# Kernel optimization log

Hardware: AMD Instinct MI355X
Metric: run time of the kernel (lower is better)

Reference implementation:

```python
import jax, jax.numpy as jnp
import numpy as np

B, N, A = 2, 4096, 5
TOPK = 30
K_RBF = 16
MAX_AA = 22
MAXREL = 32
EDGE_IN = 16 + K_RBF * 25 + 14 + 16  # 446
EDGE_FEAT = 128
PI = 3.1415926


def l2norm(v, eps=1e-12):
    n = jnp.sqrt(jnp.sum(v * v, axis=-1, keepdims=True))
    return v / jnp.maximum(n, eps)


def gather_nodes(nodes, idx):
    # nodes: (B,N,C), idx: (B,N,K) -> (B,N,K,C)
    b, n, k = idx.shape
    flat = idx.reshape(b, n * k, 1)
    out = jnp.take_along_axis(nodes, flat, axis=1)
    return out.reshape(b, n, k, nodes.shape[-1])


def quaternions(R):
    # R: (...,3,3) -> unit quaternion (...,4)
    Rxx, Ryy, Rzz = R[..., 0, 0], R[..., 1, 1], R[..., 2, 2]
    mag = 0.5 * jnp.sqrt(jnp.abs(1.0 + jnp.stack([Rxx - Ryy - Rzz, -Rxx + Ryy - Rzz, -Rxx - Ryy + Rzz], -1)) + 1e-12)
    signs = jnp.sign(jnp.stack([R[..., 2, 1] - R[..., 1, 2], R[..., 0, 2] - R[..., 2, 0], R[..., 1, 0] - R[..., 0, 1]], -1))
    xyz = signs * mag
    w = jnp.sqrt(jax.nn.relu(1.0 + Rxx + Ryy + Rzz) + 1e-12)[..., None] / 2.0
    return l2norm(jnp.concatenate([xyz, w], -1))


def setup_inputs():
    key = jax.random.key(0)
    ks = jax.random.split(key, 12)
    X = jax.random.normal(ks[0], (B, N, A, 3), jnp.float32) * 3.0
    mask = jnp.ones((B, N), jnp.float32)
    mask_atoms = jnp.ones((B, N, A), jnp.float32)
    means = jax.random.normal(ks[1], (K_RBF,), jnp.float32)
    stds = jax.random.normal(ks[2], (K_RBF,), jnp.float32)
    mul_w = jax.random.normal(ks[3], (A * A,), jnp.float32)
    bias_w = jax.random.normal(ks[4], (A * A,), jnp.float32)
    aa_pair_embed = jax.random.normal(ks[5], (MAX_AA * MAX_AA, K_RBF), jnp.float32) * 0.02
    aa_pair_embed = aa_pair_embed.at[441].set(0.0)  # padding_idx
    relpos_embed = jax.random.normal(ks[6], (2 * MAXREL + 1, 16), jnp.float32) * 0.02
    mask_embed = jax.random.normal(ks[7], (2, 16), jnp.float32) * 0.02
    W1 = jax.random.normal(ks[8], (EDGE_IN, EDGE_IN), jnp.float32) / np.sqrt(EDGE_IN)
    b1 = jnp.zeros((EDGE_IN,), jnp.float32)
    W2 = jax.random.normal(ks[9], (EDGE_IN, EDGE_FEAT), jnp.float32) / np.sqrt(EDGE_IN)
    b2 = jnp.zeros((EDGE_FEAT,), jnp.float32)
    aa = jax.random.randint(ks[10], (B, N), 0, 21, jnp.int32)
    residue_idx = jnp.tile(jnp.arange(N, dtype=jnp.int32)[None, :], (B, 1))
    chain_labels = jax.random.randint(ks[11], (B, N), 0, 2, jnp.int32)
    return dict(X=X, mask=mask, mask_atoms=mask_atoms, means=means, stds=stds, mul_w=mul_w,
                bias_w=bias_w, aa_pair_embed=aa_pair_embed, relpos_embed=relpos_embed,
                mask_embed=mask_embed, W1=W1, b1=b1, W2=W2, b2=b2, aa=aa,
                residue_idx=residue_idx, chain_labels=chain_labels)


def reference(X, mask, mask_atoms, means, stds, mul_w, bias_w, aa_pair_embed, relpos_embed,
              mask_embed, W1, b1, W2, b2, aa, residue_idx, chain_labels):
    Ca = X[:, :, 1]  # (B,N,3) C-alpha
    # ---- _dist: spatial kNN over C-alpha ----
    mask2d = mask[:, :, None] * mask[:, None, :]
    dx = Ca[:, None, :, :] - Ca[:, :, None, :]
    D = mask2d * jnp.sqrt(jnp.sum(dx * dx, -1) + 1e-6)
    D_adj = D + (1.0 - mask2d) * jnp.max(D, -1, keepdims=True)
    _, E_idx = jax.lax.top_k(-D_adj, TOPK)  # smallest distances
    mask_attend = jnp.take_along_axis(mask2d, E_idx, axis=2)  # (B,N,K)
    # ---- orientation features (local frames + quaternions) ----
    ones3 = jnp.ones((B, 1, 3), X.dtype)
    u = l2norm(jnp.concatenate([ones3, Ca[:, 1:] - Ca[:, :-1]], 1))
    b_ = l2norm(jnp.concatenate([u[:, :-1] - u[:, 1:], ones3], 1))
    n_ = l2norm(jnp.concatenate([jnp.cross(u[:, :-1], u[:, 1:]), ones3], 1))
    lf = jnp.stack([b_, n_, jnp.cross(b_, n_)], axis=2)  # (B,N,3,3)
    X_nb = gather_nodes(Ca, E_idx)                       # (B,N,K,3)
    O_nb = gather_nodes(lf.reshape(B, N, 9), E_idx).reshape(B, N, TOPK, 3, 3)
    t = X_nb - Ca[:, :, None, :]
    t = jnp.einsum('bnij,bnkj->bnki', lf, t)
    t = l2norm(t) * mask_attend[..., None]
    r = jnp.einsum('bnji,bnkjl->bnkil', lf, O_nb)  # lf^T @ O_nb
    q = quaternions(r) * mask_attend[..., None]
    O_feat = jnp.concatenate([t, q, 1.0 - 2.0 * jnp.abs(t), 1.0 - 2.0 * jnp.abs(q)], -1)  # (B,N,K,14)
    # ---- positional / chain embeddings ----
    offset = residue_idx[:, :, None] - residue_idx[:, None, :]
    offset_nb = jnp.take_along_axis(offset, E_idx, 2)
    d_chain = (chain_labels[:, :, None] == chain_labels[:, None, :]).astype(jnp.int32)
    E_chains = jnp.take_along_axis(d_chain, E_idx, 2)
    d = jnp.clip(offset_nb + MAXREL, 0, 2 * MAXREL)
    E_pos = relpos_embed[d] + mask_embed[E_chains]  # (B,N,K,16)
    # ---- GaussianLayer: aa-pair embed + atom-pair distance RBF ----
    aa_pair = aa[:, :, None] * MAX_AA + aa[:, None, :]
    aa_nb = jnp.take_along_axis(aa_pair, E_idx, 2)
    feat_aapair = aa_pair_embed[aa_nb] * mask_attend[..., None]  # (B,N,K,16)
    nbX = gather_nodes(X.reshape(B, N, A * 3), E_idx).reshape(B, N, TOPK, A, 3)
    delta = nbX[:, :, :, :, None, :] - X[:, :, None, None, :, :]  # (B,N,K,A,A,3)
    Dab = jnp.sqrt(jnp.sum(delta * delta, -1) + 1e-12)            # (B,N,K,A,A)
    et = jnp.arange(A * A).reshape(A, A)
    xg = mul_w[et] * Dab + bias_w[et]
    m_nb = gather_nodes(mask_atoms, E_idx)  # (B,N,K,A)
    xg = xg * (m_nb[..., None, :] * m_nb[..., :, None])
    std = jnp.abs(stds) + 0.01
    g = jnp.exp(-0.5 * ((xg[..., None] - means) / std) ** 2) / ((2.0 * PI) ** 0.5 * std)
    gbf = g.reshape(B, N, TOPK, A * A * K_RBF) * mask_attend[..., None]  # (B,N,K,400)
    # ---- fuse and project (NonLinear gbf_proj) ----
    E = jnp.concatenate([E_pos, gbf, O_feat, feat_aapair], -1)  # (B,N,K,446)
    h = jax.nn.gelu(E @ W1 + b1, approximate=False)
    return h @ W2 + b2  # (B,N,K,128)
```

## Files before the change

### kernel.cpp

```cpp
#include <hip/hip_runtime.h>
#include <cstdint>
#include <cstddef>

#define NN 4096
#define TOPK_ 30
#define BN_TOT 8192
#define M_TOT 245760
#define KP 448
#define HSTRIDE 136
#define EF 128

typedef unsigned short u16;
typedef unsigned int u32;
typedef __attribute__((ext_vector_type(8))) short bf16x8;
typedef __attribute__((ext_vector_type(4))) float f32x4;

__device__ __forceinline__ float b2f(u16 u){ return __uint_as_float(((u32)u)<<16); }
__device__ __forceinline__ u16 f2b(float f){
  u32 u = __float_as_uint(f);
  return (u16)((u + 0x7FFFu + ((u>>16)&1u)) >> 16);
}
__device__ __forceinline__ float ldf(const void* p, long i, int fl){
  return fl ? ((const float*)p)[i] : b2f(((const u16*)p)[i]);
}
__device__ __forceinline__ int is_f32_flag(const u16* mask){
  return (((const u32*)mask)[0] == 0x3F800000u) ? 1 : 0;
}
__device__ __forceinline__ void norm3(float x,float y,float z,float&ox,float&oy,float&oz){
  float n = sqrtf(x*x+y*y+z*z); n = fmaxf(n, 1e-12f);
  ox=x/n; oy=y/n; oz=z/n;
}
__device__ __forceinline__ float sgn(float x){ return x>0.f?1.f:(x<0.f?-1.f:0.f); }
__device__ __forceinline__ float gelu_fast(float x){
  float y = 0.70710678118654752440f * x;
  float s = fabsf(y);
  float t = __builtin_amdgcn_rcpf(fmaf(0.3275911f, s, 1.0f));
  float p = fmaf(fmaf(fmaf(fmaf(1.061405429f, t, -1.453152027f), t, 1.421413741f), t,
                 -0.284496736f), t, 0.254829592f);
  float e = __expf(-y*y);
  float erfs = fmaf(-p*t, e, 1.0f);
  float erfy = (x >= 0.f) ? erfs : -erfs;
  float hx = 0.5f*x;
  return fmaf(hx, erfy, hx);
}
__device__ __forceinline__ u32 pk_bf16(float lo, float hi){
  u32 r;
  asm("v_cvt_pk_bf16_f32 %0, %1, %2" : "=v"(r) : "v"(lo), "v"(hi));
  return r;
}
__device__ __forceinline__ void ld16(const void* p, int row, int fl, float* o){
  if (fl) {
    const float4* q = (const float4*)((const float*)p + (long)row*16);
    float4 a=q[0], b=q[1], c=q[2], d=q[3];
    o[0]=a.x; o[1]=a.y; o[2]=a.z; o[3]=a.w;
    o[4]=b.x; o[5]=b.y; o[6]=b.z; o[7]=b.w;
    o[8]=c.x; o[9]=c.y; o[10]=c.z; o[11]=c.w;
    o[12]=d.x; o[13]=d.y; o[14]=d.z; o[15]=d.w;
  } else {
    const uint4* q = (const uint4*)((const u16*)p + (long)row*16);
    uint4 a=q[0], b=q[1];
    o[0]=__uint_as_float(a.x<<16);  o[1]=__uint_as_float(a.x&0xFFFF0000u);
    o[2]=__uint_as_float(a.y<<16);  o[3]=__uint_as_float(a.y&0xFFFF0000u);
    o[4]=__uint_as_float(a.z<<16);  o[5]=__uint_as_float(a.z&0xFFFF0000u);
    o[6]=__uint_as_float(a.w<<16);  o[7]=__uint_as_float(a.w&0xFFFF0000u);
    o[8]=__uint_as_float(b.x<<16);  o[9]=__uint_as_float(b.x&0xFFFF0000u);
    o[10]=__uint_as_float(b.y<<16); o[11]=__uint_as_float(b.y&0xFFFF0000u);
    o[12]=__uint_as_float(b.z<<16); o[13]=__uint_as_float(b.z&0xFFFF0000u);
    o[14]=__uint_as_float(b.w<<16); o[15]=__uint_as_float(b.w&0xFFFF0000u);
  }
}

__global__ __launch_bounds__(256) void prep_kernel(
    const void* __restrict__ X, const u16* __restrict__ mask,
    const void* __restrict__ mask_atoms,
    const void* __restrict__ means, const void* __restrict__ stds,
    const void* __restrict__ mul_w, const void* __restrict__ bias_w,
    const void* __restrict__ W1, const void* __restrict__ b1,
    const void* __restrict__ W2, const void* __restrict__ b2,
    float* __restrict__ ca, float* __restrict__ lf,
    u16* __restrict__ W1P, u16* __restrict__ W2P,
    float* __restrict__ b1p, float* __restrict__ b2p,
    float* __restrict__ Fp, float* __restrict__ wsc)
{
  const int fl = is_f32_flag(mask);
  int idx = blockIdx.x*256 + threadIdx.x;
  if (idx < BN_TOT) {
    int i = idx & (NN-1);
    float xr[15];
    #pragma unroll
    for (int v = 0; v < 15; ++v) xr[v] = ldf(X, (long)idx*15+v, fl);
    float cax = xr[3], cay = xr[4], caz = xr[5];
    ca[idx*4+0]=cax; ca[idx*4+1]=cay; ca[idx*4+2]=caz; ca[idx*4+3]=0.f;
    {
      float mres = ldf(mask, idx, fl);
      float m0 = ldf(mask_atoms,(long)idx*5+0,fl), m1 = ldf(mask_atoms,(long)idx*5+1,fl);
      float m2 = ldf(mask_atoms,(long)idx*5+2,fl), m3 = ldf(mask_atoms,(long)idx*5+3,fl);
      float m4 = ldf(mask_atoms,(long)idx*5+4,fl);
      float4* F4 = (float4*)(Fp + (long)idx*24);
      F4[0] = make_float4(xr[0],xr[1],xr[2],xr[3]);
      F4[1] = make_float4(xr[4],xr[5],xr[6],xr[7]);
      F4[2] = make_float4(xr[8],xr[9],xr[10],xr[11]);
      F4[3] = make_float4(xr[12],xr[13],xr[14],mres);
      F4[4] = make_float4(m0,m1,m2,m3);
      F4[5] = make_float4(m4,0.f,0.f,0.f);
    }
    float bx,by,bz,nx,ny,nz;
    if (i < NN-1) {
      float uix,uiy,uiz;
      if (i==0) { norm3(1.f,1.f,1.f,uix,uiy,uiz); }
      else {
        float px=ldf(X,(long)(idx-1)*15+3,fl), py=ldf(X,(long)(idx-1)*15+4,fl), pz=ldf(X,(long)(idx-1)*15+5,fl);
        norm3(cax-px, cay-py, caz-pz, uix,uiy,uiz);
      }
      float qx=ldf(X,(long)(idx+1)*15+3,fl), qy=ldf(X,(long)(idx+1)*15+4,fl), qz=ldf(X,(long)(idx+1)*15+5,fl);
      float vx,vy,vz; norm3(qx-cax, qy-cay, qz-caz, vx,vy,vz);
      norm3(uix-vx, uiy-vy, uiz-vz, bx,by,bz);
      norm3(uiy*vz-uiz*vy, uiz*vx-uix*vz, uix*vy-uiy*vx, nx,ny,nz);
    } else {
      norm3(1.f,1.f,1.f,bx,by,bz); nx=bx; ny=by; nz=bz;
    }
    float cx = by*nz - bz*ny, cy = bz*nx - bx*nz, cz = bx*ny - by*nx;
    float* L = lf + (size_t)idx*12;
    L[0]=bx;L[1]=by;L[2]=bz;L[3]=nx;L[4]=ny;L[5]=nz;L[6]=cx;L[7]=cy;L[8]=cz;
    return;
  }
  int r1 = idx - BN_TOT;
  if (r1 < 229376) {
    int f = r1 >> 9, li = r1 & 511;
    int n0 = f / 14, kc = f - n0*14;
    int ln = li >> 3, j = li & 7;
    int n = n0*16 + (ln & 15);
    int k = kc*32 + (ln >> 4)*8 + j;
    W1P[r1] = (n < 446 && k < 446) ? (fl ? f2b(((const float*)W1)[(long)k*446 + n])
                                         : ((const u16*)W1)[(long)k*446 + n]) : (u16)0;
    return;
  }
  int r2 = r1 - 229376;
  if (r2 < 65536) {
    int f = r2 >> 9, li = r2 & 511;
    int n0 = f >> 4, kc = f & 15;
    int ln = li >> 3, j = li & 7;
    int n = n0*16 + (ln & 15);
    int k = kc*32 + (ln >> 4)*8 + j;
    W2P[r2] = (k < 446) ? (fl ? f2b(((const float*)W2)[(long)k*128 + n])
                              : ((const u16*)W2)[(long)k*128 + n]) : (u16)0;
    return;
  }
  int r3 = r2 - 65536;
  if (r3 < 512) { b1p[r3] = (r3<446)? ldf(b1, r3, fl) : 0.f; return; }
  int r4 = r3 - 512;
  if (r4 < 128) { b2p[r4] = ldf(b2, r4, fl); return; }
  int r5 = r4 - 128;
  if (r5 < 16) {
    float sd = fabsf(ldf(stds, r5, fl)) + 0.01f;
    float ri = 1.0f / sd;
    wsc[r5] = ldf(means, r5, fl);
    wsc[16 + r5] = ri;
    wsc[32 + r5] = 0.3989422804014327f * ri;
    return;
  }
  if (r5 < 41) { wsc[48 + (r5-16)] = ldf(mul_w, r5-16, fl); return; }
  if (r5 < 66) { wsc[73 + (r5-41)] = ldf(bias_w, r5-41, fl); }
}

__global__ __launch_bounds__(64) void knn_kernel(const float4* __restrict__ ca,
                                                 int* __restrict__ eidx)
{
#pragma clang fp contract(off)
  __shared__ u32 keys[64*65];
  int bi = blockIdx.x;
  int lane = threadIdx.x;
  int b = bi >> 12;
  const float4 ci = ca[bi];
  const float4* cab = ca + (b<<12);
  u32 mind = 0xFFFFFFFFu; int minj = 1<<30;
  for (int c = 0; c < 64; ++c) {
    int j = (c<<6) | lane;
    float4 cj = cab[j];
    float dx = cj.x-ci.x, dy = cj.y-ci.y, dz = cj.z-ci.z;
    float ss = dx*dx;
    ss = ss + dy*dy;
    ss = ss + dz*dz;
    float d = sqrtf(ss + 1e-6f);
    u32 db = __float_as_uint(d);
    keys[lane*65 + c] = db;
    if (db < mind) { mind = db; minj = j; }
  }
  __syncthreads();
  for (int r = 0; r < TOPK_; ++r) {
    u32 wd = mind; int wj = minj;
    #pragma unroll
    for (int off = 32; off; off >>= 1) {
      u32 od = __shfl_xor(wd, off, 64);
      int oj = __shfl_xor(wj, off, 64);
      if (od < wd || (od == wd && oj < wj)) { wd = od; wj = oj; }
    }
    if (lane == 0) eidx[bi*TOPK_ + r] = wj;
    int wl = wj & 63;
    if (lane == wl) keys[wl*65 + (wj>>6)] = 0xFFFFFFFFu;
    __syncthreads();
    u32 kv = keys[wl*65 + lane];
    int kj = (lane<<6)|wl;
    #pragma unroll
    for (int off = 32; off; off >>= 1) {
      u32 od = __shfl_xor(kv, off, 64);
      int oj = __shfl_xor(kj, off, 64);
      if (od < kv || (od == kv && oj < kj)) { kv = od; kj = oj; }
    }
    if (lane == wl) { mind = kv; minj = kj; }
  }
}

__global__ __launch_bounds__(512,2) void mega_mlp(
    const float* __restrict__ Fp, const float* __restrict__ wsc,
    const u16* __restrict__ mask,
    const void* __restrict__ aa_pe, const void* __restrict__ relpos, const void* __restrict__ mask_emb,
    const int* __restrict__ aa, const int* __restrict__ ridx, const int* __restrict__ chains,
    const int* __restrict__ eidx, const float* __restrict__ ca, const float* __restrict__ lf,
    const u16* __restrict__ W1P, const u16* __restrict__ W2P,
    const float* __restrict__ b1p, const float* __restrict__ b2p,
    void* __restrict__ C)
{
  __shared__ __align__(16) u16 Et[128*448];
  __shared__ float Dabs[128][29];
  __shared__ float maA[128];
  const int fl = is_f32_flag(mask);
  int tid = threadIdx.x;
  int lane = tid & 63, wave = tid >> 6;
  int wr = wave >> 2, wc = wave & 3;
  int rowBase = blockIdx.x * 128;

  {
    int eo = tid >> 2, q = tid & 3;
    int e = rowBase + eo;
    int bi = (int)((unsigned)e / 30u);
    int k = e - bi*30;
    int bj = ((bi >> 12) << 12) + eidx[bi*TOPK_ + k];
    const float* Fi = Fp + (long)bi*24;
    const float* Fj = Fp + (long)bj*24;
    float Xi[15];
    {
      const float4* F4 = (const float4*)Fi;
      float4 A=F4[0], B=F4[1], Cc=F4[2], D=F4[3];
      Xi[0]=A.x;Xi[1]=A.y;Xi[2]=A.z;Xi[3]=A.w;
      Xi[4]=B.x;Xi[5]=B.y;Xi[6]=B.z;Xi[7]=B.w;
      Xi[8]=Cc.x;Xi[9]=Cc.y;Xi[10]=Cc.z;Xi[11]=Cc.w;
      Xi[12]=D.x;Xi[13]=D.y;Xi[14]=D.z;
      if (q == 1) maA[eo] = D.w * Fj[15];
    }
    float4 Mj = *(const float4*)(Fj + 16);
    float  Mj4 = Fj[20];
    for (int a = q; a < 5; a += 4) {
      float xj0 = Fj[a*3+0], xj1 = Fj[a*3+1], xj2 = Fj[a*3+2];
      float mja = Fj[16+a];
      #pragma unroll
      for (int c = 0; c < 5; ++c) {
        float d0 = xj0 - Xi[c*3+0];
        float d1 = xj1 - Xi[c*3+1];
        float d2 = xj2 - Xi[c*3+2];
        float Dab = sqrtf(d0*d0 + d1*d1 + d2*d2 + 1e-12f);
        float mjc = (c==0)?Mj.x:(c==1)?Mj.y:(c==2)?Mj.z:(c==3)?Mj.w:Mj4;
        float mw = wsc[48 + a*5+c], bw = wsc[73 + a*5+c];
        Dabs[eo][a*5+c] = (mw*Dab + bw) * (mja * mjc);
      }
    }
  }

  if (tid < 128) {
    int eo = tid;
    int e = rowBase + eo;
    int bi = (int)((unsigned)e / 30u);
    int k = e - bi*30;
    int bj = ((bi >> 12) << 12) + eidx[bi*TOPK_ + k];
    float ma = Fp[(long)bi*24+15] * Fp[(long)bj*24+15];
    char* rowB = (char*)Et + eo*896;
    int xr = (eo & 7) << 4;
    {
      int d = ridx[bi] - ridx[bj] + 32; d = d < 0 ? 0 : (d > 64 ? 64 : d);
      int ch = (chains[bi] == chains[bj]) ? 1 : 0;
      float rp[16], me[16];
      ld16(relpos, d, fl, rp);
      ld16(mask_emb, ch, fl, me);
      uint4 wA, wB;
      wA.x = pk_bf16(rp[0]+me[0],  rp[1]+me[1]);
      wA.y = pk_bf16(rp[2]+me[2],  rp[3]+me[3]);
      wA.z = pk_bf16(rp[4]+me[4],  rp[5]+me[5]);
      wA.w = pk_bf16(rp[6]+me[6],  rp[7]+me[7]);
      wB.x = pk_bf16(rp[8]+me[8],  rp[9]+me[9]);
      wB.y = pk_bf16(rp[10]+me[10],rp[11]+me[11]);
      wB.z = pk_bf16(rp[12]+me[12],rp[13]+me[13]);
      wB.w = pk_bf16(rp[14]+me[14],rp[15]+me[15]);
      *(uint4*)(rowB + (0 ^ xr))  = wA;
      *(uint4*)(rowB + (16 ^ xr)) = wB;
    }
    float t0,t1,t2,q0,q1,q2,qw;
    {
      float Li[9], Lj[9];
      {
        const float4* L4 = (const float4*)(lf + (size_t)bi*12);
        float4 a=L4[0], b=L4[1], c=L4[2];
        Li[0]=a.x;Li[1]=a.y;Li[2]=a.z;Li[3]=a.w;Li[4]=b.x;Li[5]=b.y;Li[6]=b.z;Li[7]=b.w;Li[8]=c.x;
        const float4* M4 = (const float4*)(lf + (size_t)bj*12);
        float4 d=M4[0], e2=M4[1], f=M4[2];
        Lj[0]=d.x;Lj[1]=d.y;Lj[2]=d.z;Lj[3]=d.w;Lj[4]=e2.x;Lj[5]=e2.y;Lj[6]=e2.z;Lj[7]=e2.w;Lj[8]=f.x;
      }
      float4 ci = *(const float4*)(ca + bj*4);
      float4 c0 = *(const float4*)(ca + bi*4);
      float dx = ci.x-c0.x, dy = ci.y-c0.y, dz = ci.z-c0.z;
      t0 = Li[0]*dx+Li[1]*dy+Li[2]*dz;
      t1 = Li[3]*dx+Li[4]*dy+Li[5]*dz;
      t2 = Li[6]*dx+Li[7]*dy+Li[8]*dz;
      float tn = fmaxf(sqrtf(t0*t0+t1*t1+t2*t2), 1e-12f);
      t0 = t0/tn*ma; t1 = t1/tn*ma; t2 = t2/tn*ma;
      float R00=Li[0]*Lj[0]+Li[3]*Lj[3]+Li[6]*Lj[6];
      float R01=Li[0]*Lj[1]+Li[3]*Lj[4]+Li[6]*Lj[7];
      float R02=Li[0]*Lj[2]+Li[3]*Lj[5]+Li[6]*Lj[8];
      float R10=Li[1]*Lj[0]+Li[4]*Lj[3]+Li[7]*Lj[6];
      float R11=Li[1]*Lj[1]+Li[4]*Lj[4]+Li[7]*Lj[7];
      float R12=Li[1]*Lj[2]+Li[4]*Lj[5]+Li[7]*Lj[8];
      float R20=Li[2]*Lj[0]+Li[5]*Lj[3]+Li[8]*Lj[6];
      float R21=Li[2]*Lj[1]+Li[5]*Lj[4]+Li[8]*Lj[7];
      float R22=Li[2]*Lj[2]+Li[5]*Lj[5]+Li[8]*Lj[8];
      float m0 = 0.5f*sqrtf(fabsf(1.f+R00-R11-R22)+1e-12f);
      float m1 = 0.5f*sqrtf(fabsf(1.f-R00+R11-R22)+1e-12f);
      float m2 = 0.5f*sqrtf(fabsf(1.f-R00-R11+R22)+1e-12f);
      q0 = sgn(R21-R12)*m0; q1 = sgn(R02-R20)*m1; q2 = sgn(R10-R01)*m2;
      qw = 0.5f*sqrtf(fmaxf(1.f+R00+R11+R22, 0.f)+1e-12f);
      float qn = fmaxf(sqrtf(q0*q0+q1*q1+q2*q2+qw*qw), 1e-12f);
      q0 = q0/qn*ma; q1 = q1/qn*ma; q2 = q2/qn*ma; qw = qw/qn*ma;
    }
    {
      int aap = aa[bi]*22 + aa[bj];
      float av[16];
      ld16(aa_pe, aap, fl, av);
      uint4 w0, w1, w2, w3;
      w0.x = pk_bf16(t0, t1);  w0.y = pk_bf16(t2, q0);
      w0.z = pk_bf16(q1, q2);  w0.w = pk_bf16(qw, 1.f-2.f*fabsf(t0));
      w1.x = pk_bf16(1.f-2.f*fabsf(t1), 1.f-2.f*fabsf(t2));
      w1.y = pk_bf16(1.f-2.f*fabsf(q0), 1.f-2.f*fabsf(q1));
      w1.z = pk_bf16(1.f-2.f*fabsf(q2), 1.f-2.f*fabsf(qw));
      w1.w = pk_bf16(av[0]*ma, av[1]*ma);
      w2.x = pk_bf16(av[2]*ma, av[3]*ma);   w2.y = pk_bf16(av[4]*ma, av[5]*ma);
      w2.z = pk_bf16(av[6]*ma, av[7]*ma);   w2.w = pk_bf16(av[8]*ma, av[9]*ma);
      w3.x = pk_bf16(av[10]*ma, av[11]*ma); w3.y = pk_bf16(av[12]*ma, av[13]*ma);
      w3.z = pk_bf16(av[14]*ma, av[15]*ma); w3.w = 0u;
      *(uint4*)(rowB + (832 ^ xr)) = w0;
      *(uint4*)(rowB + (848 ^ xr)) = w1;
      *(uint4*)(rowB + (864 ^ xr)) = w2;
      *(uint4*)(rowB + (880 ^ xr)) = w3;
    }
  }
  __syncthreads();

  {
    float meanv[16], rinvv[16], coefv[16];
    {
      const float4* W4 = (const float4*)wsc;
      #pragma unroll
      for (int g = 0; g < 4; ++g) {
        float4 m = W4[g], r = W4[4+g], c = W4[8+g];
        meanv[g*4+0]=m.x; meanv[g*4+1]=m.y; meanv[g*4+2]=m.z; meanv[g*4+3]=m.w;
        rinvv[g*4+0]=r.x; rinvv[g*4+1]=r.y; rinvv[g*4+2]=r.z; rinvv[g*4+3]=r.w;
        coefv[g*4+0]=c.x; coefv[g*4+1]=c.y; coefv[g*4+2]=c.z; coefv[g*4+3]=c.w;
      }
    }
    #pragma unroll 1
    for (int i = 0; i < 13; ++i) {
      int G = tid + i*512;
      if (G < 6400) {
        int row = (int)((unsigned)G / 50u);
        int gp = G - row*50;
        float xg = Dabs[row][gp >> 1];
        float ma = maA[row];
        int odd = gp & 1;
        u32 w[4];
        #pragma unroll
        for (int j2 = 0; j2 < 4; ++j2) {
          float me0 = odd ? meanv[j2*2+8] : meanv[j2*2];
          float ri0 = odd ? rinvv[j2*2+8] : rinvv[j2*2];
          float co0 = odd ? coefv[j2*2+8] : coefv[j2*2];
          float me1 = odd ? meanv[j2*2+9] : meanv[j2*2+1];
          float ri1 = odd ? rinvv[j2*2+9] : rinvv[j2*2+1];
          float co1 = odd ? coefv[j2*2+9] : coefv[j2*2+1];
          float z0 = (xg - me0) * ri0;
          float z1 = (xg - me1) * ri1;
          float v0 = __expf(-0.5f*z0*z0) * co0 * ma;
          float v1 = __expf(-0.5f*z1*z1) * co1 * ma;
          w[j2] = pk_bf16(v0, v1);
        }
        uint4 W4o; W4o.x = w[0]; W4o.y = w[1]; W4o.z = w[2]; W4o.w = w[3];
        *(uint4*)((char*)Et + row*896 + ((32 + (gp<<4)) ^ ((row&7)<<4))) = W4o;
      }
    }
  }
  __syncthreads();

  u32 hpk[4][4][2][2];
  #define GEMM1_HALF(H) do {                                                      \
    f32x4 acc1h[2][4][2] = {};                                                    \
    _Pragma("unroll 1")                                                           \
    for (int t = 0; t < 7; ++t) {                                                 \
      bf16x8 af[2][4];                                                            \
      _Pragma("unroll")                                                           \
      for (int kk = 0; kk < 2; ++kk)                                              \
        _Pragma("unroll")                                                         \
        for (int r = 0; r < 4; ++r) {                                             \
          int row = wr*64 + r*16 + (lane&15);                                     \
          int s = kk*4 + (lane>>4);                                               \
          af[kk][r] = *(const bf16x8*)(Et + row*448 + t*64 + ((s ^ (row&7))<<3)); \
        }                                                                         \
      bf16x8 bg[2][2][2];                                                         \
      _Pragma("unroll")                                                           \
      for (int c = 0; c < 2; ++c)                                                 \
        _Pragma("unroll")                                                         \
        for (int cc = 0; cc < 2; ++cc)                                            \
          _Pragma("unroll")                                                       \
          for (int kk = 0; kk < 2; ++kk)                                          \
            bg[c][cc][kk] = *(const bf16x8*)(W1P +                                \
              ((((2*(H)+c)*8 + wc*2 + cc)*14 + t*2 + kk) << 9) + lane*8);         \
      _Pragma("unroll")                                                           \
      for (int c = 0; c < 2; ++c)                                                 \
        _Pragma("unroll")                                                         \
        for (int r = 0; r < 4; ++r)                                               \
          _Pragma("unroll")                                                       \
          for (int cc = 0; cc < 2; ++cc)                                          \
            _Pragma("unroll")                                                     \
            for (int kk = 0; kk < 2; ++kk)                                        \
              acc1h[c][r][cc] = __builtin_amdgcn_mfma_f32_16x16x32_bf16(          \
                  af[kk][r], bg[c][cc][kk], acc1h[c][r][cc], 0,0,0);              \
    }                                                                             \
    _Pragma("unroll")                                                             \
    for (int c = 0; c < 2; ++c)                                                   \
      _Pragma("unroll")                                                           \
      for (int r = 0; r < 4; ++r)                                                 \
        _Pragma("unroll")                                                         \
        for (int cc = 0; cc < 2; ++cc) {                                          \
          int col = wc*32 + cc*16 + (lane & 15);                                  \
          float bv = b1p[(2*(H)+c)*128 + col];                                    \
          hpk[2*(H)+c][r][cc][0] = pk_bf16(gelu_fast(acc1h[c][r][cc][0]+bv),      \
                                           gelu_fast(acc1h[c][r][cc][1]+bv));     \
          hpk[2*(H)+c][r][cc][1] = pk_bf16(gelu_fast(acc1h[c][r][cc][2]+bv),      \
                                           gelu_fast(acc1h[c][r][cc][3]+bv));     \
        }                                                                         \
  } while(0)

  GEMM1_HALF(0);
  GEMM1_HALF(1);
  #undef GEMM1_HALF

  u16* hs0 = Et;
  u16* hs1 = Et + 128*HSTRIDE;
  #define STORE_HS(cN, buf) do {                                                  \
    _Pragma("unroll")                                                             \
    for (int r = 0; r < 4; ++r) {                                                 \
      _Pragma("unroll")                                                           \
      for (int cc = 0; cc < 2; ++cc) {                                            \
        int col = wc*32 + cc*16 + (lane & 15);                                    \
        int row0 = wr*64 + r*16 + (lane>>4)*4;                                    \
        u32 p01 = hpk[cN][r][cc][0], p23 = hpk[cN][r][cc][1];                     \
        u16* hb_ = (buf) + row0*HSTRIDE + col;                                    \
        hb_[0]         = (u16)p01; hb_[HSTRIDE]   = (u16)(p01>>16);               \
        hb_[2*HSTRIDE] = (u16)p23; hb_[3*HSTRIDE] = (u16)(p23>>16);               \
      }                                                                           \
    }                                                                             \
  } while(0)

  f32x4 acc2[4][2] = {};
  __syncthreads();
  STORE_HS(0, hs0);
  __syncthreads();
  #pragma unroll
  for (int c = 0; c < 4; ++c) {
    u16* hb = (c & 1) ? hs1 : hs0;
    u16* hn = (c & 1) ? hs0 : hs1;
    if (c < 3) STORE_HS(c+1, hn);
    #pragma unroll
    for (int k2 = 0; k2 < 4; ++k2) {
      bf16x8 af2[4], bg2[2];
      #pragma unroll
      for (int r = 0; r < 4; ++r) {
        int row = wr*64 + r*16 + (lane&15);
        af2[r] = *(const bf16x8*)(hb + row*HSTRIDE + k2*32 + (lane>>4)*8);
      }
      #pragma unroll
      for (int cc = 0; cc < 2; ++cc)
        bg2[cc] = *(const bf16x8*)(W2P + ((((wc*2+cc)*16) + c*4 + k2) << 9) + lane*8);
      #pragma unroll
      for (int r = 0; r < 4; ++r)
        #pragma unroll
        for (int cc = 0; cc < 2; ++cc)
          acc2[r][cc] = __builtin_amdgcn_mfma_f32_16x16x32_bf16(af2[r], bg2[cc], acc2[r][cc], 0,0,0);
    }
    __syncthreads();
  }
  #undef STORE_HS

  const int f32out = fl;
  #pragma unroll
  for (int r = 0; r < 4; ++r) {
    #pragma unroll
    for (int cc = 0; cc < 2; ++cc) {
      int col = wc*32 + cc*16 + (lane & 15);
      float bv = b2p[col];
      #pragma unroll
      for (int g = 0; g < 4; ++g) {
        long row = (long)rowBase + wr*64 + r*16 + (lane>>4)*4 + g;
        float v = acc2[r][cc][g] + bv;
        long o = row*EF + col;
        if (f32out) ((float*)C)[o] = v;
        else        ((u16*)C)[o]  = f2b(v);
      }
    }
  }
}

extern "C" void kernel_launch(void* const* d_in, const int* in_sizes, int n_in,
                              void* d_out, int out_size, void* d_ws, size_t ws_size,
                              hipStream_t stream) {
  const void* X          = d_in[0];
  const u16* mask        = (const u16*)d_in[1];
  const void* mask_atoms = d_in[2];
  const void* means      = d_in[3];
  const void* stds       = d_in[4];
  const void* mul_w      = d_in[5];
  const void* bias_w     = d_in[6];
  const void* aa_pe      = d_in[7];
  const void* relpos     = d_in[8];
  const void* mask_emb   = d_in[9];
  const void* W1         = d_in[10];
  const void* b1         = d_in[11];
  const void* W2         = d_in[12];
  const void* b2         = d_in[13];
  const int* aa          = (const int*)d_in[14];
  const int* ridx        = (const int*)d_in[15];
  const int* chains      = (const int*)d_in[16];

  char* ws = (char*)d_ws;
  float* ca  = (float*)(ws + 0);
  float* lf  = (float*)(ws + 131072);
  int* eidx  = (int*)(ws + 524288);
  u16* W1P   = (u16*)(ws + 1507328);
  u16* W2P   = (u16*)(ws + 1966080);
  float* b1p = (float*)(ws + 2097152);
  float* b2p = (float*)(ws + 2099200);
  float* wsc = (float*)(ws + 2099712);
  float* Fp  = (float*)(ws + 2100224);

  prep_kernel<<<1187, 256, 0, stream>>>(X, mask, mask_atoms, means, stds, mul_w, bias_w,
                                        W1, b1, W2, b2, ca, lf, W1P, W2P, b1p, b2p, Fp, wsc);
  knn_kernel<<<BN_TOT, 64, 0, stream>>>((const float4*)ca, eidx);
  mega_mlp<<<M_TOT/128, 512, 0, stream>>>(Fp, wsc, mask,
                                          aa_pe, relpos, mask_emb, aa, ridx, chains,
                                          eidx, ca, lf, W1P, W2P, b1p, b2p, d_out);
}
```

Baseline: 673.3 us.

## Halve MLP row tile to 64 with 256-thread blocks and coalesced weight repack

The fused MLP kernel now processes 64 edge rows per block with 4 waves in a 2x2 arrangement instead of 128 rows with 8 waves. Each wave now covers 32 rows by 64 columns, so it loads more weight fragments per MFMA and fewer activation fragments. LDS use per block is halved, which lets more blocks fit on each CU. The prep kernel's weight repacking now indexes threads by the source (k,n) order, so global reads are coalesced and writes are scattered. The trade-off is twice as many blocks, each reading the full W1/W2 from global/L2, which raises weight traffic per output row.

```diff
diff --git a/kernel.cpp b/kernel.cpp
--- a/kernel.cpp
+++ b/kernel.cpp
@@ -9,6 +9,7 @@
 #define KP 448
 #define HSTRIDE 136
 #define EF 128
+#define BR 64
 
 typedef unsigned short u16;
 typedef unsigned int u32;
@@ -126,24 +127,22 @@
   }
   int r1 = idx - BN_TOT;
   if (r1 < 229376) {
-    int f = r1 >> 9, li = r1 & 511;
-    int n0 = f / 14, kc = f - n0*14;
-    int ln = li >> 3, j = li & 7;
-    int n = n0*16 + (ln & 15);
-    int k = kc*32 + (ln >> 4)*8 + j;
-    W1P[r1] = (n < 446 && k < 446) ? (fl ? f2b(((const float*)W1)[(long)k*446 + n])
-                                         : ((const u16*)W1)[(long)k*446 + n]) : (u16)0;
+    int k = r1 >> 9, n = r1 & 511;
+    u16 v = (n < 446 && k < 446) ? (fl ? f2b(((const float*)W1)[(long)k*446 + n])
+                                       : ((const u16*)W1)[(long)k*446 + n]) : (u16)0;
+    int frag = (n >> 4)*14 + (k >> 5);
+    int li = ((n & 15) + 16*((k & 31) >> 3))*8 + (k & 7);
+    W1P[(frag << 9) + li] = v;
     return;
   }
   int r2 = r1 - 229376;
   if (r2 < 65536) {
-    int f = r2 >> 9, li = r2 & 511;
-    int n0 = f >> 4, kc = f & 15;
-    int ln = li >> 3, j = li & 7;
-    int n = n0*16 + (ln & 15);
-    int k = kc*32 + (ln >> 4)*8 + j;
-    W2P[r2] = (k < 446) ? (fl ? f2b(((const float*)W2)[(long)k*128 + n])
-                              : ((const u16*)W2)[(long)k*128 + n]) : (u16)0;
+    int k = r2 >> 7, n = r2 & 127;
+    u16 v = (k < 446) ? (fl ? f2b(((const float*)W2)[(long)k*128 + n])
+                            : ((const u16*)W2)[(long)k*128 + n]) : (u16)0;
+    int frag = (n >> 4)*16 + (k >> 5);
+    int li = ((n & 15) + 16*((k & 31) >> 3))*8 + (k & 7);
+    W2P[(frag << 9) + li] = v;
     return;
   }
   int r3 = r2 - 65536;
@@ -211,7 +210,7 @@
   }
 }
 
-__global__ __launch_bounds__(512,2) void mega_mlp(
+__global__ __launch_bounds__(256,2) void mega_mlp(
     const float* __restrict__ Fp, const float* __restrict__ wsc,
     const u16* __restrict__ mask,
     const void* __restrict__ aa_pe, const void* __restrict__ relpos, const void* __restrict__ mask_emb,
@@ -221,14 +220,14 @@
     const float* __restrict__ b1p, const float* __restrict__ b2p,
     void* __restrict__ C)
 {
-  __shared__ __align__(16) u16 Et[128*448];
-  __shared__ float Dabs[128][29];
-  __shared__ float maA[128];
+  __shared__ __align__(16) u16 Et[BR*448];
+  __shared__ float Dabs[BR][29];
+  __shared__ float maA[BR];
   const int fl = is_f32_flag(mask);
   int tid = threadIdx.x;
   int lane = tid & 63, wave = tid >> 6;
-  int wr = wave >> 2, wc = wave & 3;
-  int rowBase = blockIdx.x * 128;
+  int wr = wave >> 1, wc = wave & 1;
+  int rowBase = blockIdx.x * BR;
 
   {
     int eo = tid >> 2, q = tid & 3;
@@ -266,7 +265,7 @@
     }
   }
 
-  if (tid < 128) {
+  if (tid < BR) {
     int eo = tid;
     int e = rowBase + eo;
     int bi = (int)((unsigned)e / 30u);
@@ -295,32 +294,27 @@
     }
     float t0,t1,t2,q0,q1,q2,qw;
     {
-      float Li[9], Lj[9];
-      {
-        const float4* L4 = (const float4*)(lf + (size_t)bi*12);
-        float4 a=L4[0], b=L4[1], c=L4[2];
-        Li[0]=a.x;Li[1]=a.y;Li[2]=a.z;Li[3]=a.w;Li[4]=b.x;Li[5]=b.y;Li[6]=b.z;Li[7]=b.w;Li[8]=c.x;
-        const float4* M4 = (const float4*)(lf + (size_t)bj*12);
-        float4 d=M4[0], e2=M4[1], f=M4[2];
-        Lj[0]=d.x;Lj[1]=d.y;Lj[2]=d.z;Lj[3]=d.w;Lj[4]=e2.x;Lj[5]=e2.y;Lj[6]=e2.z;Lj[7]=e2.w;Lj[8]=f.x;
-      }
-      float4 ci = *(const float4*)(ca + bj*4);
-      float4 c0 = *(const float4*)(ca + bi*4);
-      float dx = ci.x-c0.x, dy = ci.y-c0.y, dz = ci.z-c0.z;
-      t0 = Li[0]*dx+Li[1]*dy+Li[2]*dz;
-      t1 = Li[3]*dx+Li[4]*dy+Li[5]*dz;
-      t2 = Li[6]*dx+Li[7]*dy+Li[8]*dz;
+      const float4* L4i = (const float4*)(lf + (size_t)bi*12);
+      float4 a0=L4i[0], a1=L4i[1], a2=L4i[2];
+      const float4* L4j = (const float4*)(lf + (size_t)bj*12);
+      float4 b0=L4j[0], b1v=L4j[1], b2v=L4j[2];
+      float4 cj4 = *(const float4*)(ca + bj*4);
+      float4 ci4 = *(const float4*)(ca + bi*4);
+      float dx = cj4.x-ci4.x, dy = cj4.y-ci4.y, dz = cj4.z-ci4.z;
+      t0 = a0.x*dx + a0.y*dy + a0.z*dz;
+      t1 = a0.w*dx + a1.x*dy + a1.y*dz;
+      t2 = a1.z*dx + a1.w*dy + a2.x*dz;
       float tn = fmaxf(sqrtf(t0*t0+t1*t1+t2*t2), 1e-12f);
       t0 = t0/tn*ma; t1 = t1/tn*ma; t2 = t2/tn*ma;
-      float R00=Li[0]*Lj[0]+Li[3]*Lj[3]+Li[6]*Lj[6];
-      float R01=Li[0]*Lj[1]+Li[3]*Lj[4]+Li[6]*Lj[7];
-      float R02=Li[0]*Lj[2]+Li[3]*Lj[5]+Li[6]*Lj[8];
-      float R10=Li[1]*Lj[0]+Li[4]*Lj[3]+Li[7]*Lj[6];
-      float R11=Li[1]*Lj[1]+Li[4]*Lj[4]+Li[7]*Lj[7];
-      float R12=Li[1]*Lj[2]+Li[4]*Lj[5]+Li[7]*Lj[8];
-      float R20=Li[2]*Lj[0]+Li[5]*Lj[3]+Li[8]*Lj[6];
-      float R21=Li[2]*Lj[1]+Li[5]*Lj[4]+Li[8]*Lj[7];
-      float R22=Li[2]*Lj[2]+Li[5]*Lj[5]+Li[8]*Lj[8];
+      float R00 = a0.x*b0.x + a0.w*b0.w + a1.z*b1v.z;
+      float R01 = a0.x*b0.y + a0.w*b1v.x + a1.z*b1v.w;
+      float R02 = a0.x*b0.z + a0.w*b1v.y + a1.z*b2v.x;
+      float R10 = a0.y*b0.x + a1.x*b0.w + a1.w*b1v.z;
+      float R11 = a0.y*b0.y + a1.x*b1v.x + a1.w*b1v.w;
+      float R12 = a0.y*b0.z + a1.x*b1v.y + a1.w*b2v.x;
+      float R20 = a0.z*b0.x + a1.y*b0.w + a2.x*b1v.z;
+      float R21 = a0.z*b0.y + a1.y*b1v.x + a2.x*b1v.w;
+      float R22 = a0.z*b0.z + a1.y*b1v.y + a2.x*b2v.x;
       float m0 = 0.5f*sqrtf(fabsf(1.f+R00-R11-R22)+1e-12f);
       float m1 = 0.5f*sqrtf(fabsf(1.f-R00+R11-R22)+1e-12f);
       float m2 = 0.5f*sqrtf(fabsf(1.f-R00-R11+R22)+1e-12f);
@@ -366,8 +360,8 @@
     }
     #pragma unroll 1
     for (int i = 0; i < 13; ++i) {
-      int G = tid + i*512;
-      if (G < 6400) {
+      int G = tid + i*256;
+      if (G < 3200) {
         int row = (int)((unsigned)G / 50u);
         int gp = G - row*50;
         float xg = Dabs[row][gp >> 1];
@@ -395,47 +389,46 @@
   }
   __syncthreads();
 
-  u32 hpk[4][4][2][2];
+  u32 hpk[4][2][4][2];
   #define GEMM1_HALF(H) do {                                                      \
-    f32x4 acc1h[2][4][2] = {};                                                    \
+    f32x4 acc1h[2][2][4] = {};                                                    \
     _Pragma("unroll 1")                                                           \
     for (int t = 0; t < 7; ++t) {                                                 \
-      bf16x8 af[2][4];                                                            \
+      bf16x8 af[2][2];                                                            \
       _Pragma("unroll")                                                           \
       for (int kk = 0; kk < 2; ++kk)                                              \
         _Pragma("unroll")                                                         \
-        for (int r = 0; r < 4; ++r) {                                             \
-          int row = wr*64 + r*16 + (lane&15);                                     \
+        for (int r = 0; r < 2; ++r) {                                             \
+          int row = wr*32 + r*16 + (lane&15);                                     \
           int s = kk*4 + (lane>>4);                                               \
           af[kk][r] = *(const bf16x8*)(Et + row*448 + t*64 + ((s ^ (row&7))<<3)); \
         }                                                                         \
-      bf16x8 bg[2][2][2];                                                         \
       _Pragma("unroll")                                                           \
-      for (int c = 0; c < 2; ++c)                                                 \
+      for (int c = 0; c < 2; ++c) {                                               \
+        bf16x8 bg[4][2];                                                          \
         _Pragma("unroll")                                                         \
-        for (int cc = 0; cc < 2; ++cc)                                            \
+        for (int cc = 0; cc < 4; ++cc)                                            \
           _Pragma("unroll")                                                       \
           for (int kk = 0; kk < 2; ++kk)                                          \
-            bg[c][cc][kk] = *(const bf16x8*)(W1P +                                \
-              ((((2*(H)+c)*8 + wc*2 + cc)*14 + t*2 + kk) << 9) + lane*8);         \
-      _Pragma("unroll")                                                           \
-      for (int c = 0; c < 2; ++c)                                                 \
+            bg[cc][kk] = *(const bf16x8*)(W1P +                                   \
+              ((((2*(H)+c)*8 + wc*4 + cc)*14 + t*2 + kk) << 9) + lane*8);         \
         _Pragma("unroll")                                                         \
-        for (int r = 0; r < 4; ++r)                                               \
+        for (int r = 0; r < 2; ++r)                                               \
           _Pragma("unroll")                                                       \
-          for (int cc = 0; cc < 2; ++cc)                                          \
+          for (int cc = 0; cc < 4; ++cc)                                          \
             _Pragma("unroll")                                                     \
             for (int kk = 0; kk < 2; ++kk)                                        \
               acc1h[c][r][cc] = __builtin_amdgcn_mfma_f32_16x16x32_bf16(          \
-                  af[kk][r], bg[c][cc][kk], acc1h[c][r][cc], 0,0,0);              \
+                  af[kk][r], bg[cc][kk], acc1h[c][r][cc], 0,0,0);                 \
+      }                                                                           \
     }                                                                             \
     _Pragma("unroll")                                                             \
     for (int c = 0; c < 2; ++c)                                                   \
       _Pragma("unroll")                                                           \
-      for (int r = 0; r < 4; ++r)                                                 \
+      for (int r = 0; r < 2; ++r)                                                 \
         _Pragma("unroll")                                                         \
-        for (int cc = 0; cc < 2; ++cc) {                                          \
-          int col = wc*32 + cc*16 + (lane & 15);                                  \
+        for (int cc = 0; cc < 4; ++cc) {                                          \
+          int col = wc*64 + cc*16 + (lane & 15);                                  \
           float bv = b1p[(2*(H)+c)*128 + col];                                    \
           hpk[2*(H)+c][r][cc][0] = pk_bf16(gelu_fast(acc1h[c][r][cc][0]+bv),      \
                                            gelu_fast(acc1h[c][r][cc][1]+bv));     \
@@ -449,14 +442,14 @@
   #undef GEMM1_HALF
 
   u16* hs0 = Et;
-  u16* hs1 = Et + 128*HSTRIDE;
+  u16* hs1 = Et + BR*HSTRIDE;
   #define STORE_HS(cN, buf) do {                                                  \
     _Pragma("unroll")                                                             \
-    for (int r = 0; r < 4; ++r) {                                                 \
+    for (int r = 0; r < 2; ++r) {                                                 \
       _Pragma("unroll")                                                           \
-      for (int cc = 0; cc < 2; ++cc) {                                            \
-        int col = wc*32 + cc*16 + (lane & 15);                                    \
-        int row0 = wr*64 + r*16 + (lane>>4)*4;                                    \
+      for (int cc = 0; cc < 4; ++cc) {                                            \
+        int col = wc*64 + cc*16 + (lane & 15);                                    \
+        int row0 = wr*32 + r*16 + (lane>>4)*4;                                    \
         u32 p01 = hpk[cN][r][cc][0], p23 = hpk[cN][r][cc][1];                     \
         u16* hb_ = (buf) + row0*HSTRIDE + col;                                    \
         hb_[0]         = (u16)p01; hb_[HSTRIDE]   = (u16)(p01>>16);               \
@@ -465,7 +458,7 @@
     }                                                                             \
   } while(0)
 
-  f32x4 acc2[4][2] = {};
+  f32x4 acc2[2][4] = {};
   __syncthreads();
   STORE_HS(0, hs0);
   __syncthreads();
@@ -476,19 +469,19 @@
     if (c < 3) STORE_HS(c+1, hn);
     #pragma unroll
     for (int k2 = 0; k2 < 4; ++k2) {
-      bf16x8 af2[4], bg2[2];
+      bf16x8 af2[2], bg2[4];
       #pragma unroll
-      for (int r = 0; r < 4; ++r) {
-        int row = wr*64 + r*16 + (lane&15);
+      for (int r = 0; r < 2; ++r) {
+        int row = wr*32 + r*16 + (lane&15);
         af2[r] = *(const bf16x8*)(hb + row*HSTRIDE + k2*32 + (lane>>4)*8);
       }
       #pragma unroll
-      for (int cc = 0; cc < 2; ++cc)
-        bg2[cc] = *(const bf16x8*)(W2P + ((((wc*2+cc)*16) + c*4 + k2) << 9) + lane*8);
+      for (int cc = 0; cc < 4; ++cc)
+        bg2[cc] = *(const bf16x8*)(W2P + ((((wc*4+cc)*16) + c*4 + k2) << 9) + lane*8);
       #pragma unroll
-      for (int r = 0; r < 4; ++r)
+      for (int r = 0; r < 2; ++r)
         #pragma unroll
-        for (int cc = 0; cc < 2; ++cc)
+        for (int cc = 0; cc < 4; ++cc)
           acc2[r][cc] = __builtin_amdgcn_mfma_f32_16x16x32_bf16(af2[r], bg2[cc], acc2[r][cc], 0,0,0);
     }
     __syncthreads();
@@ -497,14 +490,14 @@
 
   const int f32out = fl;
   #pragma unroll
-  for (int r = 0; r < 4; ++r) {
+  for (int r = 0; r < 2; ++r) {
     #pragma unroll
-    for (int cc = 0; cc < 2; ++cc) {
-      int col = wc*32 + cc*16 + (lane & 15);
+    for (int cc = 0; cc < 4; ++cc) {
+      int col = wc*64 + cc*16 + (lane & 15);
       float bv = b2p[col];
       #pragma unroll
       for (int g = 0; g < 4; ++g) {
-        long row = (long)rowBase + wr*64 + r*16 + (lane>>4)*4 + g;
+        long row = (long)rowBase + wr*32 + r*16 + (lane>>4)*4 + g;
         float v = acc2[r][cc][g] + bv;
         long o = row*EF + col;
         if (f32out) ((float*)C)[o] = v;
@@ -549,7 +542,7 @@
   prep_kernel<<<1187, 256, 0, stream>>>(X, mask, mask_atoms, means, stds, mul_w, bias_w,
                                         W1, b1, W2, b2, ca, lf, W1P, W2P, b1p, b2p, Fp, wsc);
   knn_kernel<<<BN_TOT, 64, 0, stream>>>((const float4*)ca, eidx);
-  mega_mlp<<<M_TOT/128, 512, 0, stream>>>(Fp, wsc, mask,
-                                          aa_pe, relpos, mask_emb, aa, ridx, chains,
-                                          eidx, ca, lf, W1P, W2P, b1p, b2p, d_out);
-}
+  mega_mlp<<<M_TOT/BR, 256, 0, stream>>>(Fp, wsc, mask,
+                                         aa_pe, relpos, mask_emb, aa, ridx, chains,
+                                         eidx, ca, lf, W1P, W2P, b1p, b2p, d_out);
+}
```

After: 660.2 us. Within noise of the previous version (-1.9%).
